# Performance work log

Measured on AMD Instinct MI355X. Metric: run time of the kernel, lower is better.

The kernel has to match this reference:

```python
import jax, jax.numpy as jnp
import numpy as np

B, C, H, W = 32, 384, 64, 64
M, R = 64, 16  # token_count, factor_r


def setup_inputs() -> dict:
    key = jax.random.key(0)
    k1, k2, k3, k4 = jax.random.split(key, 4)
    x = jax.random.normal(k1, (B, C, H, W), dtype=jnp.float32)
    # 1x1 conv == per-pixel linear map C -> R
    Vw = jax.random.normal(k2, (R, C), dtype=jnp.float32) * (1.0 / np.sqrt(C))
    Vb = jax.random.normal(k3, (R,), dtype=jnp.float32) * 0.01
    U = jax.random.normal(k4, (M, R), dtype=jnp.float32) * 0.02
    return {"x": x, "Vw": Vw, "Vb": Vb, "U": U}


def reference(x, Vw, Vb, U):
    b, c, h, w = x.shape
    n = h * w
    x_flat = x.reshape(b, c, n)                       # [B,C,N]
    # 1x1 conv projection: [B,R,N]
    V = jnp.einsum('rc,bcn->brn', Vw, x_flat) + Vb[None, :, None]
    # low-rank bilinear logits: [B,M,N]
    L = jnp.einsum('mr,brn->bmn', U, V)
    # softmax over token dim (axis=1), matching F.softmax(L, dim=1)
    S = jax.nn.softmax(L, axis=1)
    # pooled tokens: [B,C,M]
    T = jnp.einsum('bcn,bmn->bcm', x_flat, S)
    return (T, S)
```

## Files before the change

kernel.cpp:

```cpp
#include <hip/hip_runtime.h>
#include <hip/hip_bf16.h>

#define B_ 32
#define C_ 384
#define N_ 4096
#define M_ 64
#define R_ 16

typedef __attribute__((ext_vector_type(8))) short short8;
typedef __attribute__((ext_vector_type(4))) float f32x4;
typedef __attribute__((ext_vector_type(4))) int i32x4;

static __device__ __forceinline__ unsigned short f2bf(float f) {
    union { float f; unsigned u; } v; v.f = f;
    unsigned r = v.u + 0x7fffu + ((v.u >> 16) & 1u);
    return (unsigned short)(r >> 16);
}

__global__ __launch_bounds__(256) void k_w2(
    const float* __restrict__ Vw, const float* __restrict__ Vb,
    const float* __restrict__ U, unsigned short* __restrict__ W2,
    float* __restrict__ b2)
{
    __shared__ float vws[16 * 384];
    __shared__ float vbs[16];
    const int t = threadIdx.x;

    #pragma unroll
    for (int j = 0; j < 6; ++j)
        ((float4*)vws)[t + j * 256] = ((const float4*)Vw)[t + j * 256];
    if (t < 16) vbs[t] = Vb[t];
    __syncthreads();

    const int m  = blockIdx.x * 8 + (t >> 5);
    const int cg = t & 31;
    float u[R_];
    #pragma unroll
    for (int r = 0; r < R_; ++r) u[r] = U[m * R_ + r];
    if (cg == 0) {
        float a = 0.f;
        #pragma unroll
        for (int r = 0; r < R_; ++r) a = fmaf(u[r], vbs[r], a);
        b2[m] = a;
    }
    #pragma unroll
    for (int j = 0; j < 6; ++j) {
        const int c = cg * 2 + j * 64;
        float a0 = 0.f, a1 = 0.f;
        #pragma unroll
        for (int r = 0; r < R_; ++r) {
            float2 vv = *(const float2*)(vws + r * C_ + c);
            a0 = fmaf(u[r], vv.x, a0);
            a1 = fmaf(u[r], vv.y, a1);
        }
        unsigned pk = (unsigned)f2bf(a0) | ((unsigned)f2bf(a1) << 16);
        *(unsigned*)&W2[m * C_ + c] = pk;
    }
}

__global__ __launch_bounds__(512, 2) void k_fused(
    const float* __restrict__ x, const unsigned short* __restrict__ W2,
    const float* __restrict__ b2g, float* __restrict__ S, float* __restrict__ T)
{
    __shared__ unsigned short xcn[C_ * 64];
    __shared__ unsigned short xts[2][64][68];
    __shared__ unsigned short slds[M_ * 64];
    __shared__ float wred[2][4][64];

    const int t    = threadIdx.x;
    const int lane = t & 63;
    const int col  = lane & 15;
    const int q    = lane >> 4;
    const int l31  = lane & 31;
    const int l5   = lane >> 5;
    const int w    = t >> 6;
    const int g    = w >> 1;
    const int h    = w & 1;

    const int b  = blockIdx.x >> 4;
    const int nq = blockIdx.x & 15;

    float bias[4];
    #pragma unroll
    for (int r = 0; r < 4; ++r) bias[r] = b2g[g * 16 + q * 4 + r];

    f32x4 acc2[3][4];
    #pragma unroll
    for (int ci = 0; ci < 3; ++ci)
        #pragma unroll
        for (int mt = 0; mt < 4; ++mt) acc2[ci][mt] = (f32x4){0.f, 0.f, 0.f, 0.f};

    const float* xb = x + (size_t)b * C_ * N_ + nq * 256 + 2 * l31;
    const unsigned short* wrow = W2 + (g * 16 + col) * C_ + q * 8;

    float2 xv[2][4];
    short8 afr[2][2];

    auto ISSUE = [&](float2 (&dst)[4], int subp, int kcp) {
        const float* xp = xb + (size_t)(kcp * 64 + w * 8 + l5 * 4) * N_ + subp * 64;
        #pragma unroll
        for (int j = 0; j < 4; ++j)
            dst[j] = *(const float2*)(xp + (size_t)j * N_);
    };

    auto WLOAD = [&](short8 (&dst)[2], int kcp) {
        dst[0] = *(const short8*)(wrow + kcp * 64);
        dst[1] = *(const short8*)(wrow + kcp * 64 + 32);
    };

    auto CONVERT = [&](float2 (&v)[4], int kcp, int buf) {
        unsigned short bx[4], by[4];
        #pragma unroll
        for (int j = 0; j < 4; ++j) { bx[j] = f2bf(v[j].x); by[j] = f2bf(v[j].y); }
        #pragma unroll
        for (int j = 0; j < 4; ++j) {
            int c = kcp * 64 + w * 8 + l5 * 4 + j;
            unsigned pk = (unsigned)bx[j] | ((unsigned)by[j] << 16);
            *(unsigned*)((char*)xcn + c * 128 + ((4 * l31) ^ ((c & 7) << 4))) = pk;
        }
        int cl = w * 8 + l5 * 4;
        int2 pa, pb;
        pa.x = (int)((unsigned)bx[0] | ((unsigned)bx[1] << 16));
        pa.y = (int)((unsigned)bx[2] | ((unsigned)bx[3] << 16));
        pb.x = (int)((unsigned)by[0] | ((unsigned)by[1] << 16));
        pb.y = (int)((unsigned)by[2] | ((unsigned)by[3] << 16));
        *(int2*)&xts[buf][2 * l31][cl]     = pa;
        *(int2*)&xts[buf][2 * l31 + 1][cl] = pb;
    };

    ISSUE(xv[0], 0, 0);
    WLOAD(afr[0], 0);

    for (int sub = 0; sub < 4; ++sub) {
        f32x4 acc1[2];
        acc1[0] = (f32x4){0.f, 0.f, 0.f, 0.f};
        acc1[1] = (f32x4){0.f, 0.f, 0.f, 0.f};

        #pragma unroll
        for (int kc = 0; kc < 6; ++kc) {
            if (kc < 5) {
                ISSUE(xv[(kc + 1) & 1], sub, kc + 1);
                WLOAD(afr[(kc + 1) & 1], kc + 1);
            } else {
                if (sub < 3) ISSUE(xv[0], sub + 1, 0);
                WLOAD(afr[0], 0);
            }

            CONVERT(xv[kc & 1], kc, kc & 1);
            __syncthreads();

            #pragma unroll
            for (int ks = 0; ks < 2; ++ks) {
                short8 bfr[2];
                #pragma unroll
                for (int nt = 0; nt < 2; ++nt)
                    bfr[nt] = *(const short8*)&xts[kc & 1][h * 32 + nt * 16 + col][ks * 32 + q * 8];
                #pragma unroll
                for (int nt = 0; nt < 2; ++nt)
                    acc1[nt] = __builtin_amdgcn_mfma_f32_16x16x32_bf16(
                        afr[kc & 1][ks], bfr[nt], acc1[nt], 0, 0, 0);
            }
        }

        float mxl[2], scl[2];
        #pragma unroll
        for (int nt = 0; nt < 2; ++nt) {
            float mx = -3.4e38f;
            #pragma unroll
            for (int r = 0; r < 4; ++r) {
                float vv = acc1[nt][r] + bias[r];
                acc1[nt][r] = vv;
                mx = fmaxf(mx, vv);
            }
            mx = fmaxf(mx, __shfl_xor(mx, 16, 64));
            mx = fmaxf(mx, __shfl_xor(mx, 32, 64));
            float s = 0.f;
            #pragma unroll
            for (int r = 0; r < 4; ++r) {
                float e = __expf(acc1[nt][r] - mx);
                acc1[nt][r] = e;
                s += e;
            }
            s += __shfl_xor(s, 16, 64);
            s += __shfl_xor(s, 32, 64);
            mxl[nt] = mx;
            if (q == 0) {
                int n = h * 32 + nt * 16 + col;
                wred[0][g][n] = mx;
                wred[1][g][n] = s;
            }
        }
        __syncthreads();

        #pragma unroll
        for (int nt = 0; nt < 2; ++nt) {
            int n = h * 32 + nt * 16 + col;
            float m0 = wred[0][0][n], m1 = wred[0][1][n];
            float m2 = wred[0][2][n], m3 = wred[0][3][n];
            float M  = fmaxf(fmaxf(m0, m1), fmaxf(m2, m3));
            float tot = wred[1][0][n] * __expf(m0 - M) + wred[1][1][n] * __expf(m1 - M)
                      + wred[1][2][n] * __expf(m2 - M) + wred[1][3][n] * __expf(m3 - M);
            scl[nt] = __expf(mxl[nt] - M) / tot;
        }

        float* Sp = S + (size_t)(b * M_ + g * 16 + q * 4) * N_ + nq * 256 + sub * 64;
        #pragma unroll
        for (int nt = 0; nt < 2; ++nt) {
            int n = h * 32 + nt * 16 + col;
            #pragma unroll
            for (int r = 0; r < 4; ++r) {
                float p = acc1[nt][r] * scl[nt];
                Sp[(size_t)r * N_ + n] = p;
                int m = g * 16 + q * 4 + r;
                *(unsigned short*)((char*)slds + m * 128 + ((2 * n) ^ ((m & 7) << 4))) = f2bf(p);
            }
        }
        __syncthreads();

        #pragma unroll
        for (int ks = 0; ks < 2; ++ks) {
            short8 a2[3], bsf[4];
            #pragma unroll
            for (int ci = 0; ci < 3; ++ci) {
                int c = w * 48 + ci * 16 + col;
                a2[ci] = *(const short8*)((char*)xcn + c * 128 +
                                          ((ks * 64 + q * 16) ^ ((c & 7) << 4)));
            }
            #pragma unroll
            for (int mt = 0; mt < 4; ++mt) {
                int m = mt * 16 + col;
                bsf[mt] = *(const short8*)((char*)slds + m * 128 +
                                           ((ks * 64 + q * 16) ^ ((m & 7) << 4)));
            }
            #pragma unroll
            for (int ci = 0; ci < 3; ++ci)
                #pragma unroll
                for (int mt = 0; mt < 4; ++mt)
                    acc2[ci][mt] = __builtin_amdgcn_mfma_f32_16x16x32_bf16(
                        a2[ci], bsf[mt], acc2[ci][mt], 0, 0, 0);
        }
        __syncthreads();
    }

    float* Tb = T + (size_t)b * C_ * M_;
    #pragma unroll
    for (int ci = 0; ci < 3; ++ci) {
        int c = w * 48 + ci * 16 + q * 4;
        #pragma unroll
        for (int mt = 0; mt < 4; ++mt)
            #pragma unroll
            for (int r = 0; r < 4; ++r)
                atomicAdd(&Tb[(size_t)(c + r) * M_ + mt * 16 + col], acc2[ci][mt][r]);
    }
}

extern "C" void kernel_launch(void* const* d_in, const int* in_sizes, int n_in,
                              void* d_out, int out_size, void* d_ws, size_t ws_size,
                              hipStream_t stream) {
    const float* x  = (const float*)d_in[0];
    const float* Vw = (const float*)d_in[1];
    const float* Vb = (const float*)d_in[2];
    const float* U  = (const float*)d_in[3];
    float* T = (float*)d_out;
    float* S = (float*)d_out + (size_t)B_ * C_ * M_;

    unsigned short* W2 = (unsigned short*)d_ws;
    float* b2 = (float*)((char*)d_ws + 64 * 384 * 2);

    hipMemsetAsync(T, 0, (size_t)B_ * C_ * M_ * sizeof(float), stream);
    k_w2<<<dim3(8), dim3(256), 0, stream>>>(Vw, Vb, U, W2, b2);
    k_fused<<<dim3(512), dim3(512), 0, stream>>>(x, W2, b2, S, T);
}
```

Measured before the change: 327.1 us.

## Deepen x prefetch to three stages and replace atomics with partial-sum reduction

The x global loads are now prefetched three k-chunks ahead through a triple register buffer instead of two, giving memory latency more time to be hidden behind the MFMA work. The float-to-bf16 packing uses the intrinsic paired conversion. The final T accumulation no longer uses atomicAdd. Each of the 16 N-slices writes its own partial tile to workspace, and a separate reduce kernel sums them, which also removes the memset. The cost is more register pressure from the extra buffer, about 25 MB of extra partial-sum traffic, and one more kernel launch.

```diff
diff --git a/kernel.cpp b/kernel.cpp
--- a/kernel.cpp
+++ b/kernel.cpp
@@ -15,6 +15,11 @@
     union { float f; unsigned u; } v; v.f = f;
     unsigned r = v.u + 0x7fffu + ((v.u >> 16) & 1u);
     return (unsigned short)(r >> 16);
+}
+
+static __device__ __forceinline__ unsigned pk2(float lo, float hi) {
+    __hip_bfloat162 t = __float22bfloat162_rn(float2{lo, hi});
+    return *reinterpret_cast<unsigned*>(&t);
 }
 
 __global__ __launch_bounds__(256) void k_w2(
@@ -60,7 +65,7 @@
 
 __global__ __launch_bounds__(512, 2) void k_fused(
     const float* __restrict__ x, const unsigned short* __restrict__ W2,
-    const float* __restrict__ b2g, float* __restrict__ S, float* __restrict__ T)
+    const float* __restrict__ b2g, float* __restrict__ S, float* __restrict__ Tp)
 {
     __shared__ unsigned short xcn[C_ * 64];
     __shared__ unsigned short xts[2][64][68];
@@ -93,7 +98,7 @@
     const float* xb = x + (size_t)b * C_ * N_ + nq * 256 + 2 * l31;
     const unsigned short* wrow = W2 + (g * 16 + col) * C_ + q * 8;
 
-    float2 xv[2][4];
+    float2 xv[3][4];
     short8 afr[2][2];
 
     auto ISSUE = [&](float2 (&dst)[4], int subp, int kcp) {
@@ -109,26 +114,25 @@
     };
 
     auto CONVERT = [&](float2 (&v)[4], int kcp, int buf) {
-        unsigned short bx[4], by[4];
-        #pragma unroll
-        for (int j = 0; j < 4; ++j) { bx[j] = f2bf(v[j].x); by[j] = f2bf(v[j].y); }
         #pragma unroll
         for (int j = 0; j < 4; ++j) {
             int c = kcp * 64 + w * 8 + l5 * 4 + j;
-            unsigned pk = (unsigned)bx[j] | ((unsigned)by[j] << 16);
-            *(unsigned*)((char*)xcn + c * 128 + ((4 * l31) ^ ((c & 7) << 4))) = pk;
+            *(unsigned*)((char*)xcn + c * 128 + ((4 * l31) ^ ((c & 7) << 4))) =
+                pk2(v[j].x, v[j].y);
         }
         int cl = w * 8 + l5 * 4;
         int2 pa, pb;
-        pa.x = (int)((unsigned)bx[0] | ((unsigned)bx[1] << 16));
-        pa.y = (int)((unsigned)bx[2] | ((unsigned)bx[3] << 16));
-        pb.x = (int)((unsigned)by[0] | ((unsigned)by[1] << 16));
-        pb.y = (int)((unsigned)by[2] | ((unsigned)by[3] << 16));
+        pa.x = (int)pk2(v[0].x, v[1].x);
+        pa.y = (int)pk2(v[2].x, v[3].x);
+        pb.x = (int)pk2(v[0].y, v[1].y);
+        pb.y = (int)pk2(v[2].y, v[3].y);
         *(int2*)&xts[buf][2 * l31][cl]     = pa;
         *(int2*)&xts[buf][2 * l31 + 1][cl] = pb;
     };
 
     ISSUE(xv[0], 0, 0);
+    ISSUE(xv[1], 0, 1);
+    ISSUE(xv[2], 0, 2);
     WLOAD(afr[0], 0);
 
     for (int sub = 0; sub < 4; ++sub) {
@@ -138,15 +142,13 @@
 
         #pragma unroll
         for (int kc = 0; kc < 6; ++kc) {
-            if (kc < 5) {
-                ISSUE(xv[(kc + 1) & 1], sub, kc + 1);
-                WLOAD(afr[(kc + 1) & 1], kc + 1);
-            } else {
-                if (sub < 3) ISSUE(xv[0], sub + 1, 0);
-                WLOAD(afr[0], 0);
-            }
-
-            CONVERT(xv[kc & 1], kc, kc & 1);
+            CONVERT(xv[kc % 3], kc, kc & 1);
+            const int nk = kc + 3;
+            if (nk < 6)       ISSUE(xv[kc % 3], sub, nk);
+            else if (sub < 3) ISSUE(xv[kc % 3], sub + 1, nk - 6);
+            if (kc < 5) WLOAD(afr[(kc + 1) & 1], kc + 1);
+            else        WLOAD(afr[0], 0);
+
             __syncthreads();
 
             #pragma unroll
@@ -242,7 +244,7 @@
         __syncthreads();
     }
 
-    float* Tb = T + (size_t)b * C_ * M_;
+    float* Tb = Tp + ((size_t)nq * B_ + b) * C_ * M_;
     #pragma unroll
     for (int ci = 0; ci < 3; ++ci) {
         int c = w * 48 + ci * 16 + q * 4;
@@ -250,8 +252,22 @@
         for (int mt = 0; mt < 4; ++mt)
             #pragma unroll
             for (int r = 0; r < 4; ++r)
-                atomicAdd(&Tb[(size_t)(c + r) * M_ + mt * 16 + col], acc2[ci][mt][r]);
-    }
+                Tb[(size_t)(c + r) * M_ + mt * 16 + col] = acc2[ci][mt][r];
+    }
+}
+
+__global__ __launch_bounds__(256) void k_reduce(
+    const float* __restrict__ Tp, float* __restrict__ T)
+{
+    const size_t SZ = (size_t)B_ * C_ * M_;
+    size_t i = (size_t)(blockIdx.x * 256 + threadIdx.x) * 4;
+    f32x4 s = *(const f32x4*)&Tp[i];
+    #pragma unroll
+    for (int p = 1; p < 16; ++p) {
+        f32x4 v = *(const f32x4*)&Tp[p * SZ + i];
+        s.x += v.x; s.y += v.y; s.z += v.z; s.w += v.w;
+    }
+    *(f32x4*)&T[i] = s;
 }
 
 extern "C" void kernel_launch(void* const* d_in, const int* in_sizes, int n_in,
@@ -266,8 +282,9 @@
 
     unsigned short* W2 = (unsigned short*)d_ws;
     float* b2 = (float*)((char*)d_ws + 64 * 384 * 2);
-
-    hipMemsetAsync(T, 0, (size_t)B_ * C_ * M_ * sizeof(float), stream);
+    float* Tp = (float*)((char*)d_ws + (1 << 16));
+
     k_w2<<<dim3(8), dim3(256), 0, stream>>>(Vw, Vb, U, W2, b2);
-    k_fused<<<dim3(512), dim3(512), 0, stream>>>(x, W2, b2, S, T);
-}
+    k_fused<<<dim3(512), dim3(512), 0, stream>>>(x, W2, b2, S, Tp);
+    k_reduce<<<dim3(768), dim3(256), 0, stream>>>(Tp, T);
+}
```

Result: faster. 315.2 us (-3.6%).
